# Optimization experiments

Measured on AMD Instinct MI355X. Metric: run time of the kernel, lower is better.

Reference implementation:

```python
import jax, jax.numpy as jnp
import numpy as np

N = 8192      # agent_num
F = 128       # feature dim
P = 16        # persona dim
E = 262144    # edges (N * avg_degree 32)


def setup_inputs() -> dict:
    key = jax.random.key(0)
    ks = jax.random.split(key, 10)
    return {
        "feature": jax.random.normal(ks[0], (N, F), dtype=jnp.float32),
        "next_feature": jax.random.normal(ks[1], (N, F), dtype=jnp.float32),
        "persona_t": jax.random.uniform(ks[2], (N, P), dtype=jnp.float32),
        "alpha": jax.random.normal(ks[3], (P,), dtype=jnp.float32),
        "beta": jax.random.normal(ks[4], (P,), dtype=jnp.float32),
        "gamma": jax.random.normal(ks[5], (P,), dtype=jnp.float32),
        "act_src": jax.random.randint(ks[6], (E,), 0, N, dtype=jnp.int32),
        "act_dst": jax.random.randint(ks[7], (E,), 0, N, dtype=jnp.int32),
        "edge_src": jax.random.randint(ks[8], (E,), 0, N, dtype=jnp.int32),
        "edge_dst": jax.random.randint(ks[9], (E,), 0, N, dtype=jnp.int32),
    }


def _row_l2_normalize(x):
    # norm_func: divide each row by its L2 norm (scatter-add of squares in torch)
    norms = jnp.sqrt(jnp.sum(x * x, axis=1, keepdims=True))
    return x / norms


def reference(feature, next_feature, persona_t, alpha, beta, gamma,
              act_src, act_dst, edge_src, edge_dst):
    n, f = feature.shape

    # ---- impact (gamma) path: adj_sim_self(next_action, old - new) ----
    diff = feature - next_feature                           # [N, F]
    # hadamard(adj, diff @ diff.T): only dot products on action edges
    impact_vals = jnp.sum(diff[act_src] * diff[act_dst], axis=1) / f   # [E]
    gamma_row = persona_t @ gamma                            # [N] persona-weighted gamma
    reward_impact = impact_vals * gamma_row[act_src]         # row-wise multiply

    # ---- similarity (alpha) path: adj_sim(next_action, norm(next_feature)) ----
    # step() normalizes next_feature, then adj_sim normalizes again (idempotent)
    nf = _row_l2_normalize(_row_l2_normalize(next_feature))  # [N, F]
    sim_vals = jnp.sum(nf[act_src] * nf[act_dst], axis=1)    # [E] cosine sims on edges
    alpha_row = persona_t @ alpha                            # [N]
    reward_sim = sim_vals * alpha_row[act_src]

    # ---- cost (beta) path: old edges (binary) * persona_beta broadcast over rows ----
    beta_row = persona_t @ beta                              # [N]
    reward_cost = beta_row[edge_src]                         # [E] (edge value = 1)

    # ---- reward = reward_sim - reward_cost + reward_impact on the union of supports ----
    reward = jnp.zeros((n, n), dtype=feature.dtype)
    reward = reward.at[act_src, act_dst].add(reward_sim + reward_impact)
    reward = reward.at[edge_src, edge_dst].add(-reward_cost)
    return reward
```

## Files before the change

### kernel.cpp

```cpp
#include <hip/hip_runtime.h>
#include <hip/hip_fp16.h>

#define N_AGENTS 8192
#define FDIM 128
#define PDIM 16
#define NEDGES 262144
#define CAP 128
#define OVERCAP 4096

typedef float floatx4 __attribute__((ext_vector_type(4)));
typedef int   intx2   __attribute__((ext_vector_type(2)));

__global__ __launch_bounds__(256) void row_prep_k(
        const float* __restrict__ feature,
        const float* __restrict__ next_feature,
        const float* __restrict__ persona,
        const float* __restrict__ alpha,
        const float* __restrict__ beta,
        const float* __restrict__ gamma,
        __half2* __restrict__ T2,
        float2* __restrict__ scale,
        float* __restrict__ brow,
        int* __restrict__ cnt,
        int* __restrict__ ocnt) {
    int row  = (blockIdx.x * blockDim.x + threadIdx.x) >> 6;
    int lane = threadIdx.x & 63;
    if (blockIdx.x == 0 && threadIdx.x == 0) *ocnt = 0;
    if (row >= N_AGENTS) return;

    const float2* f2 = (const float2*)(feature      + (size_t)row * FDIM);
    const float2* n2 = (const float2*)(next_feature + (size_t)row * FDIM);
    float2 f  = f2[lane];
    float2 nx = n2[lane];

    float2 d = make_float2(f.x - nx.x, f.y - nx.y);
    float ss = nx.x * nx.x + nx.y * nx.y;

    float pa = 0.f, pb = 0.f, pg = 0.f;
    if (lane < PDIM) {
        float p = persona[(size_t)row * PDIM + lane];
        pa = p * alpha[lane];
        pb = p * beta[lane];
        pg = p * gamma[lane];
    }

    #pragma unroll
    for (int off = 32; off > 0; off >>= 1) {
        ss += __shfl_xor(ss, off);
        pa += __shfl_xor(pa, off);
        pb += __shfl_xor(pb, off);
        pg += __shfl_xor(pg, off);
    }

    float inv = 1.0f / sqrtf(ss);
    __half2* trow = T2 + (size_t)row * 128;
    trow[lane]      = __float22half2_rn(make_float2(nx.x * inv, nx.y * inv));
    trow[64 + lane] = __float22half2_rn(d);

    if (lane == 0) {
        scale[row] = make_float2(pa, pg * (1.0f / FDIM));
        brow[row]  = pb;
        cnt[row]   = 0;
    }
}

__device__ inline float dot8(float4 a, float4 b) {
    const __half2* ha = (const __half2*)&a;
    const __half2* hb = (const __half2*)&b;
    float s = 0.f;
    #pragma unroll
    for (int j = 0; j < 4; ++j) {
        float2 fa = __half22float2(ha[j]);
        float2 fb = __half22float2(hb[j]);
        s += fa.x * fb.x + fa.y * fb.y;
    }
    return s;
}

__device__ inline void push_rec(int s, int d, float val,
                                int* cnt, intx2* bins,
                                int* ocnt, int4* olist) {
    int pos = atomicAdd(&cnt[s], 1);
    if (pos < CAP) {
        intx2 rec;
        rec.x = d;
        rec.y = __float_as_int(val);
        __builtin_nontemporal_store(rec, &bins[(size_t)s * CAP + pos]);
    } else {
        int op = atomicAdd(ocnt, 1);
        if (op < OVERCAP) olist[op] = make_int4(s, d, __float_as_int(val), 0);
    }
}

#define ACT_BLOCKS ((NEDGES * 16) / 256)
#define COST_BLOCKS (NEDGES / 256)
__global__ __launch_bounds__(256) void edge_bin_k(
        const int* __restrict__ asrc,
        const int* __restrict__ adst,
        const int* __restrict__ esrc,
        const int* __restrict__ edst,
        const __half* __restrict__ T,
        const float2* __restrict__ scale,
        const float* __restrict__ brow,
        int* __restrict__ cnt,
        intx2* __restrict__ bins,
        int* __restrict__ ocnt,
        int4* __restrict__ olist) {
    int b = blockIdx.x;
    if (b < ACT_BLOCKS) {
        int gid    = b * 256 + threadIdx.x;
        int e      = gid >> 4;
        int lane16 = gid & 15;
        int s = asrc[e];
        int d = adst[e];
        const float4* ts = (const float4*)(T + (size_t)s * 256);
        const float4* td = (const float4*)(T + (size_t)d * 256);
        int i0 = lane16 * 2;
        float acc = dot8(ts[i0], td[i0]) + dot8(ts[i0 + 1], td[i0 + 1]);
        acc += __shfl_xor(acc, 1, 16);
        acc += __shfl_xor(acc, 2, 16);
        acc += __shfl_xor(acc, 4, 16);
        float other = __shfl_xor(acc, 8, 16);
        if (lane16 == 0) {
            float2 sc = scale[s];
            float val = acc * sc.x + other * sc.y;
            push_rec(s, d, val, cnt, bins, ocnt, olist);
        }
    } else {
        int e = (b - ACT_BLOCKS) * 256 + threadIdx.x;
        int s = esrc[e];
        push_rec(s, edst[e], -brow[s], cnt, bins, ocnt, olist);
    }
}

__global__ __launch_bounds__(256) void row_assemble_k(
        const int* __restrict__ cnt,
        const intx2* __restrict__ bins,
        float* __restrict__ out) {
    __shared__ float rowbuf[N_AGENTS];
    int r   = blockIdx.x;
    int tid = threadIdx.x;

    floatx4* rb4 = (floatx4*)rowbuf;
    floatx4 z = (floatx4)0.f;
    #pragma unroll
    for (int i = 0; i < 8; ++i)
        rb4[tid + i * 256] = z;
    __syncthreads();

    int c = cnt[r];
    c = c < CAP ? c : CAP;
    for (int i = tid; i < c; i += 256) {
        intx2 rec = bins[(size_t)r * CAP + i];
        atomicAdd(&rowbuf[rec.x], __int_as_float(rec.y));
    }
    __syncthreads();

    floatx4* dst = (floatx4*)(out + (size_t)r * N_AGENTS);
    #pragma unroll
    for (int i = 0; i < 8; ++i)
        __builtin_nontemporal_store(rb4[tid + i * 256], &dst[tid + i * 256]);
}

__global__ __launch_bounds__(256) void overflow_k(
        const int* __restrict__ ocnt,
        const int4* __restrict__ olist,
        float* __restrict__ out) {
    int n = *ocnt;
    n = n < OVERCAP ? n : OVERCAP;
    for (int i = threadIdx.x; i < n; i += 256) {
        int4 rec = olist[i];
        atomicAdd(out + (size_t)rec.x * N_AGENTS + rec.y, __int_as_float(rec.z));
    }
}

extern "C" void kernel_launch(void* const* d_in, const int* in_sizes, int n_in,
                              void* d_out, int out_size, void* d_ws, size_t ws_size,
                              hipStream_t stream) {
    const float* feature      = (const float*)d_in[0];
    const float* next_feature = (const float*)d_in[1];
    const float* persona      = (const float*)d_in[2];
    const float* alpha        = (const float*)d_in[3];
    const float* beta         = (const float*)d_in[4];
    const float* gamma        = (const float*)d_in[5];
    const int*   act_src      = (const int*)d_in[6];
    const int*   act_dst      = (const int*)d_in[7];
    const int*   edge_src     = (const int*)d_in[8];
    const int*   edge_dst     = (const int*)d_in[9];

    float* out = (float*)d_out;

    char* ws = (char*)d_ws;
    __half* T     = (__half*)ws;                 ws += (size_t)N_AGENTS * 256 * sizeof(__half);
    float2* scale = (float2*)ws;                 ws += (size_t)N_AGENTS * sizeof(float2);
    float*  brow  = (float*)ws;                  ws += (size_t)N_AGENTS * sizeof(float);
    int*    cnt   = (int*)ws;                    ws += (size_t)N_AGENTS * sizeof(int);
    intx2*  bins  = (intx2*)ws;                  ws += (size_t)N_AGENTS * CAP * sizeof(intx2);
    int*    ocnt  = (int*)ws;                    ws += 16;
    int4*   olist = (int4*)ws;

    row_prep_k<<<N_AGENTS / 4, 256, 0, stream>>>(
        feature, next_feature, persona, alpha, beta, gamma,
        (__half2*)T, scale, brow, cnt, ocnt);

    edge_bin_k<<<ACT_BLOCKS + COST_BLOCKS, 256, 0, stream>>>(
        act_src, act_dst, edge_src, edge_dst,
        T, scale, brow, cnt, bins, ocnt, olist);

    row_assemble_k<<<N_AGENTS, 256, 0, stream>>>(cnt, bins, out);

    overflow_k<<<1, 256, 0, stream>>>(ocnt, olist, out);
}
```

Baseline: 338.2 us.

## Replace per-row binning and assembly with memset plus direct global atomics

Drops the per-source-row bucket scheme (counters, capped bins, overflow list, shared-memory row assembly). Edge values are now computed into a flat array, the 256MB output is cleared with hipMemsetAsync, and a scatter kernel atomically adds each action and cost edge straight into global memory. This removes the bin write/read traffic and the shared-memory assembly pass. In exchange it relies on the memset's write bandwidth and on scattered global float atomics over a large matrix.

```diff
diff --git a/kernel.cpp b/kernel.cpp
--- a/kernel.cpp
+++ b/kernel.cpp
@@ -5,11 +5,8 @@
 #define FDIM 128
 #define PDIM 16
 #define NEDGES 262144
-#define CAP 128
-#define OVERCAP 4096
 
 typedef float floatx4 __attribute__((ext_vector_type(4)));
-typedef int   intx2   __attribute__((ext_vector_type(2)));
 
 __global__ __launch_bounds__(256) void row_prep_k(
         const float* __restrict__ feature,
@@ -20,12 +17,9 @@
         const float* __restrict__ gamma,
         __half2* __restrict__ T2,
         float2* __restrict__ scale,
-        float* __restrict__ brow,
-        int* __restrict__ cnt,
-        int* __restrict__ ocnt) {
+        float* __restrict__ brow) {
     int row  = (blockIdx.x * blockDim.x + threadIdx.x) >> 6;
     int lane = threadIdx.x & 63;
-    if (blockIdx.x == 0 && threadIdx.x == 0) *ocnt = 0;
     if (row >= N_AGENTS) return;
 
     const float2* f2 = (const float2*)(feature      + (size_t)row * FDIM);
@@ -60,7 +54,6 @@
     if (lane == 0) {
         scale[row] = make_float2(pa, pg * (1.0f / FDIM));
         brow[row]  = pb;
-        cnt[row]   = 0;
     }
 }
 
@@ -77,100 +70,47 @@
     return s;
 }
 
-__device__ inline void push_rec(int s, int d, float val,
-                                int* cnt, intx2* bins,
-                                int* ocnt, int4* olist) {
-    int pos = atomicAdd(&cnt[s], 1);
-    if (pos < CAP) {
-        intx2 rec;
-        rec.x = d;
-        rec.y = __float_as_int(val);
-        __builtin_nontemporal_store(rec, &bins[(size_t)s * CAP + pos]);
-    } else {
-        int op = atomicAdd(ocnt, 1);
-        if (op < OVERCAP) olist[op] = make_int4(s, d, __float_as_int(val), 0);
+#define ACT_BLOCKS ((NEDGES * 16) / 256)
+__global__ __launch_bounds__(256) void act_val_k(
+        const int* __restrict__ asrc,
+        const int* __restrict__ adst,
+        const __half* __restrict__ T,
+        const float2* __restrict__ scale,
+        float* __restrict__ actval) {
+    int gid    = blockIdx.x * 256 + threadIdx.x;
+    int e      = gid >> 4;
+    int lane16 = gid & 15;
+    int s = asrc[e];
+    int d = adst[e];
+    const float4* ts = (const float4*)(T + (size_t)s * 256);
+    const float4* td = (const float4*)(T + (size_t)d * 256);
+    int i0 = lane16 * 2;
+    float acc = dot8(ts[i0], td[i0]) + dot8(ts[i0 + 1], td[i0 + 1]);
+    acc += __shfl_xor(acc, 1, 16);
+    acc += __shfl_xor(acc, 2, 16);
+    acc += __shfl_xor(acc, 4, 16);
+    float other = __shfl_xor(acc, 8, 16);
+    if (lane16 == 0) {
+        float2 sc = scale[s];
+        actval[e] = acc * sc.x + other * sc.y;
     }
 }
 
-#define ACT_BLOCKS ((NEDGES * 16) / 256)
-#define COST_BLOCKS (NEDGES / 256)
-__global__ __launch_bounds__(256) void edge_bin_k(
+__global__ __launch_bounds__(256) void scatter_k(
         const int* __restrict__ asrc,
         const int* __restrict__ adst,
+        const float* __restrict__ actval,
         const int* __restrict__ esrc,
         const int* __restrict__ edst,
-        const __half* __restrict__ T,
-        const float2* __restrict__ scale,
         const float* __restrict__ brow,
-        int* __restrict__ cnt,
-        intx2* __restrict__ bins,
-        int* __restrict__ ocnt,
-        int4* __restrict__ olist) {
-    int b = blockIdx.x;
-    if (b < ACT_BLOCKS) {
-        int gid    = b * 256 + threadIdx.x;
-        int e      = gid >> 4;
-        int lane16 = gid & 15;
-        int s = asrc[e];
-        int d = adst[e];
-        const float4* ts = (const float4*)(T + (size_t)s * 256);
-        const float4* td = (const float4*)(T + (size_t)d * 256);
-        int i0 = lane16 * 2;
-        float acc = dot8(ts[i0], td[i0]) + dot8(ts[i0 + 1], td[i0 + 1]);
-        acc += __shfl_xor(acc, 1, 16);
-        acc += __shfl_xor(acc, 2, 16);
-        acc += __shfl_xor(acc, 4, 16);
-        float other = __shfl_xor(acc, 8, 16);
-        if (lane16 == 0) {
-            float2 sc = scale[s];
-            float val = acc * sc.x + other * sc.y;
-            push_rec(s, d, val, cnt, bins, ocnt, olist);
-        }
+        float* __restrict__ out) {
+    int t = blockIdx.x * 256 + threadIdx.x;
+    if (t < NEDGES) {
+        atomicAdd(out + (size_t)asrc[t] * N_AGENTS + adst[t], actval[t]);
     } else {
-        int e = (b - ACT_BLOCKS) * 256 + threadIdx.x;
+        int e = t - NEDGES;
         int s = esrc[e];
-        push_rec(s, edst[e], -brow[s], cnt, bins, ocnt, olist);
-    }
-}
-
-__global__ __launch_bounds__(256) void row_assemble_k(
-        const int* __restrict__ cnt,
-        const intx2* __restrict__ bins,
-        float* __restrict__ out) {
-    __shared__ float rowbuf[N_AGENTS];
-    int r   = blockIdx.x;
-    int tid = threadIdx.x;
-
-    floatx4* rb4 = (floatx4*)rowbuf;
-    floatx4 z = (floatx4)0.f;
-    #pragma unroll
-    for (int i = 0; i < 8; ++i)
-        rb4[tid + i * 256] = z;
-    __syncthreads();
-
-    int c = cnt[r];
-    c = c < CAP ? c : CAP;
-    for (int i = tid; i < c; i += 256) {
-        intx2 rec = bins[(size_t)r * CAP + i];
-        atomicAdd(&rowbuf[rec.x], __int_as_float(rec.y));
-    }
-    __syncthreads();
-
-    floatx4* dst = (floatx4*)(out + (size_t)r * N_AGENTS);
-    #pragma unroll
-    for (int i = 0; i < 8; ++i)
-        __builtin_nontemporal_store(rb4[tid + i * 256], &dst[tid + i * 256]);
-}
-
-__global__ __launch_bounds__(256) void overflow_k(
-        const int* __restrict__ ocnt,
-        const int4* __restrict__ olist,
-        float* __restrict__ out) {
-    int n = *ocnt;
-    n = n < OVERCAP ? n : OVERCAP;
-    for (int i = threadIdx.x; i < n; i += 256) {
-        int4 rec = olist[i];
-        atomicAdd(out + (size_t)rec.x * N_AGENTS + rec.y, __int_as_float(rec.z));
+        atomicAdd(out + (size_t)s * N_AGENTS + edst[e], -brow[s]);
     }
 }
 
@@ -191,23 +131,20 @@
     float* out = (float*)d_out;
 
     char* ws = (char*)d_ws;
-    __half* T     = (__half*)ws;                 ws += (size_t)N_AGENTS * 256 * sizeof(__half);
-    float2* scale = (float2*)ws;                 ws += (size_t)N_AGENTS * sizeof(float2);
-    float*  brow  = (float*)ws;                  ws += (size_t)N_AGENTS * sizeof(float);
-    int*    cnt   = (int*)ws;                    ws += (size_t)N_AGENTS * sizeof(int);
-    intx2*  bins  = (intx2*)ws;                  ws += (size_t)N_AGENTS * CAP * sizeof(intx2);
-    int*    ocnt  = (int*)ws;                    ws += 16;
-    int4*   olist = (int4*)ws;
+    __half* T      = (__half*)ws;   ws += (size_t)N_AGENTS * 256 * sizeof(__half);
+    float2* scale  = (float2*)ws;   ws += (size_t)N_AGENTS * sizeof(float2);
+    float*  brow   = (float*)ws;    ws += (size_t)N_AGENTS * sizeof(float);
+    float*  actval = (float*)ws;
 
     row_prep_k<<<N_AGENTS / 4, 256, 0, stream>>>(
         feature, next_feature, persona, alpha, beta, gamma,
-        (__half2*)T, scale, brow, cnt, ocnt);
+        (__half2*)T, scale, brow);
 
-    edge_bin_k<<<ACT_BLOCKS + COST_BLOCKS, 256, 0, stream>>>(
-        act_src, act_dst, edge_src, edge_dst,
-        T, scale, brow, cnt, bins, ocnt, olist);
+    act_val_k<<<ACT_BLOCKS, 256, 0, stream>>>(
+        act_src, act_dst, T, scale, actval);
 
-    row_assemble_k<<<N_AGENTS, 256, 0, stream>>>(cnt, bins, out);
+    hipMemsetAsync(out, 0, (size_t)N_AGENTS * N_AGENTS * sizeof(float), stream);
 
-    overflow_k<<<1, 256, 0, stream>>>(ocnt, olist, out);
+    scatter_k<<<(2 * NEDGES) / 256, 256, 0, stream>>>(
+        act_src, act_dst, actval, edge_src, edge_dst, brow, out);
 }
```

Measured after the change: 357.0 us. +5.6%, slower.

## Move edge dot products into row assembly with split index-only bins

Applied to the files above, without the earlier changes.

Binning now stores only destination indices, in separate bins for action edges and cost edges, so the scatter pass no longer gathers features. The dot products run in the row-assembly kernel, where the source row of T is loaded once per block into registers and reused for all of that row's edges. The aim is to cut redundant source-row gathers and shrink bin records from 8 to 4 bytes. The cost is more work in the assembly kernel and a more complex overflow kernel that recomputes dot products on a single block.

```diff
diff --git a/kernel.cpp b/kernel.cpp
--- a/kernel.cpp
+++ b/kernel.cpp
@@ -9,7 +9,6 @@
 #define OVERCAP 4096
 
 typedef float floatx4 __attribute__((ext_vector_type(4)));
-typedef int   intx2   __attribute__((ext_vector_type(2)));
 
 __global__ __launch_bounds__(256) void row_prep_k(
         const float* __restrict__ feature,
@@ -21,7 +20,8 @@
         __half2* __restrict__ T2,
         float2* __restrict__ scale,
         float* __restrict__ brow,
-        int* __restrict__ cnt,
+        int* __restrict__ cntA,
+        int* __restrict__ cntC,
         int* __restrict__ ocnt) {
     int row  = (blockIdx.x * blockDim.x + threadIdx.x) >> 6;
     int lane = threadIdx.x & 63;
@@ -60,7 +60,8 @@
     if (lane == 0) {
         scale[row] = make_float2(pa, pg * (1.0f / FDIM));
         brow[row]  = pb;
-        cnt[row]   = 0;
+        cntA[row]  = 0;
+        cntC[row]  = 0;
     }
 }
 
@@ -77,83 +78,78 @@
     return s;
 }
 
-__device__ inline void push_rec(int s, int d, float val,
-                                int* cnt, intx2* bins,
-                                int* ocnt, int4* olist) {
-    int pos = atomicAdd(&cnt[s], 1);
-    if (pos < CAP) {
-        intx2 rec;
-        rec.x = d;
-        rec.y = __float_as_int(val);
-        __builtin_nontemporal_store(rec, &bins[(size_t)s * CAP + pos]);
-    } else {
-        int op = atomicAdd(ocnt, 1);
-        if (op < OVERCAP) olist[op] = make_int4(s, d, __float_as_int(val), 0);
-    }
-}
-
-#define ACT_BLOCKS ((NEDGES * 16) / 256)
-#define COST_BLOCKS (NEDGES / 256)
 __global__ __launch_bounds__(256) void edge_bin_k(
         const int* __restrict__ asrc,
         const int* __restrict__ adst,
         const int* __restrict__ esrc,
         const int* __restrict__ edst,
+        int* __restrict__ cntA,
+        int* __restrict__ cntC,
+        int* __restrict__ binsA,
+        int* __restrict__ binsC,
+        int* __restrict__ ocnt,
+        int4* __restrict__ olist) {
+    int t = blockIdx.x * 256 + threadIdx.x;
+    if (t < NEDGES) {
+        int s = asrc[t];
+        int d = adst[t];
+        int pos = atomicAdd(&cntA[s], 1);
+        if (pos < CAP) binsA[(size_t)s * CAP + pos] = d;
+        else { int op = atomicAdd(ocnt, 1); if (op < OVERCAP) olist[op] = make_int4(s, d, 0, 0); }
+    } else {
+        int e = t - NEDGES;
+        int s = esrc[e];
+        int d = edst[e];
+        int pos = atomicAdd(&cntC[s], 1);
+        if (pos < CAP) binsC[(size_t)s * CAP + pos] = d;
+        else { int op = atomicAdd(ocnt, 1); if (op < OVERCAP) olist[op] = make_int4(s, d, 1, 0); }
+    }
+}
+
+__global__ __launch_bounds__(256) void row_assemble_k(
+        const int* __restrict__ cntA,
+        const int* __restrict__ binsA,
+        const int* __restrict__ cntC,
+        const int* __restrict__ binsC,
         const __half* __restrict__ T,
         const float2* __restrict__ scale,
         const float* __restrict__ brow,
-        int* __restrict__ cnt,
-        intx2* __restrict__ bins,
-        int* __restrict__ ocnt,
-        int4* __restrict__ olist) {
-    int b = blockIdx.x;
-    if (b < ACT_BLOCKS) {
-        int gid    = b * 256 + threadIdx.x;
-        int e      = gid >> 4;
-        int lane16 = gid & 15;
-        int s = asrc[e];
-        int d = adst[e];
-        const float4* ts = (const float4*)(T + (size_t)s * 256);
+        float* __restrict__ out) {
+    __shared__ float rowbuf[N_AGENTS];
+    int r   = blockIdx.x;
+    int tid = threadIdx.x;
+
+    floatx4* rb4 = (floatx4*)rowbuf;
+    floatx4 z = (floatx4)0.f;
+    #pragma unroll
+    for (int i = 0; i < 8; ++i)
+        rb4[tid + i * 256] = z;
+
+    int grp    = tid >> 4;
+    int lane16 = tid & 15;
+    int i0     = lane16 * 2;
+    const float4* tr = (const float4*)(T + (size_t)r * 256);
+    float4 tsA = tr[i0];
+    float4 tsB = tr[i0 + 1];
+    float2 sc  = scale[r];
+    float  br  = brow[r];
+    int cA = cntA[r]; cA = cA < CAP ? cA : CAP;
+    int cC = cntC[r]; cC = cC < CAP ? cC : CAP;
+    __syncthreads();
+
+    for (int i = grp; i < cA; i += 16) {
+        int d = binsA[(size_t)r * CAP + i];
         const float4* td = (const float4*)(T + (size_t)d * 256);
-        int i0 = lane16 * 2;
-        float acc = dot8(ts[i0], td[i0]) + dot8(ts[i0 + 1], td[i0 + 1]);
+        float acc = dot8(tsA, td[i0]) + dot8(tsB, td[i0 + 1]);
         acc += __shfl_xor(acc, 1, 16);
         acc += __shfl_xor(acc, 2, 16);
         acc += __shfl_xor(acc, 4, 16);
         float other = __shfl_xor(acc, 8, 16);
-        if (lane16 == 0) {
-            float2 sc = scale[s];
-            float val = acc * sc.x + other * sc.y;
-            push_rec(s, d, val, cnt, bins, ocnt, olist);
-        }
-    } else {
-        int e = (b - ACT_BLOCKS) * 256 + threadIdx.x;
-        int s = esrc[e];
-        push_rec(s, edst[e], -brow[s], cnt, bins, ocnt, olist);
-    }
-}
-
-__global__ __launch_bounds__(256) void row_assemble_k(
-        const int* __restrict__ cnt,
-        const intx2* __restrict__ bins,
-        float* __restrict__ out) {
-    __shared__ float rowbuf[N_AGENTS];
-    int r   = blockIdx.x;
-    int tid = threadIdx.x;
-
-    floatx4* rb4 = (floatx4*)rowbuf;
-    floatx4 z = (floatx4)0.f;
-    #pragma unroll
-    for (int i = 0; i < 8; ++i)
-        rb4[tid + i * 256] = z;
-    __syncthreads();
-
-    int c = cnt[r];
-    c = c < CAP ? c : CAP;
-    for (int i = tid; i < c; i += 256) {
-        intx2 rec = bins[(size_t)r * CAP + i];
-        atomicAdd(&rowbuf[rec.x], __int_as_float(rec.y));
-    }
+        if (lane16 == 0)
+            atomicAdd(&rowbuf[d], acc * sc.x + other * sc.y);
+    }
+    for (int i = tid; i < cC; i += 256)
+        atomicAdd(&rowbuf[binsC[(size_t)r * CAP + i]], -br);
     __syncthreads();
 
     floatx4* dst = (floatx4*)(out + (size_t)r * N_AGENTS);
@@ -165,12 +161,34 @@
 __global__ __launch_bounds__(256) void overflow_k(
         const int* __restrict__ ocnt,
         const int4* __restrict__ olist,
+        const __half* __restrict__ T,
+        const float2* __restrict__ scale,
+        const float* __restrict__ brow,
         float* __restrict__ out) {
     int n = *ocnt;
     n = n < OVERCAP ? n : OVERCAP;
-    for (int i = threadIdx.x; i < n; i += 256) {
+    int grp    = threadIdx.x >> 4;
+    int lane16 = threadIdx.x & 15;
+    int i0     = lane16 * 2;
+    for (int i = grp; i < n; i += 16) {
         int4 rec = olist[i];
-        atomicAdd(out + (size_t)rec.x * N_AGENTS + rec.y, __int_as_float(rec.z));
+        if (rec.z) {
+            if (lane16 == 0)
+                atomicAdd(out + (size_t)rec.x * N_AGENTS + rec.y, -brow[rec.x]);
+        } else {
+            const float4* ts = (const float4*)(T + (size_t)rec.x * 256);
+            const float4* td = (const float4*)(T + (size_t)rec.y * 256);
+            float acc = dot8(ts[i0], td[i0]) + dot8(ts[i0 + 1], td[i0 + 1]);
+            acc += __shfl_xor(acc, 1, 16);
+            acc += __shfl_xor(acc, 2, 16);
+            acc += __shfl_xor(acc, 4, 16);
+            float other = __shfl_xor(acc, 8, 16);
+            if (lane16 == 0) {
+                float2 sc = scale[rec.x];
+                atomicAdd(out + (size_t)rec.x * N_AGENTS + rec.y,
+                          acc * sc.x + other * sc.y);
+            }
+        }
     }
 }
 
@@ -191,23 +209,26 @@
     float* out = (float*)d_out;
 
     char* ws = (char*)d_ws;
-    __half* T     = (__half*)ws;                 ws += (size_t)N_AGENTS * 256 * sizeof(__half);
-    float2* scale = (float2*)ws;                 ws += (size_t)N_AGENTS * sizeof(float2);
-    float*  brow  = (float*)ws;                  ws += (size_t)N_AGENTS * sizeof(float);
-    int*    cnt   = (int*)ws;                    ws += (size_t)N_AGENTS * sizeof(int);
-    intx2*  bins  = (intx2*)ws;                  ws += (size_t)N_AGENTS * CAP * sizeof(intx2);
-    int*    ocnt  = (int*)ws;                    ws += 16;
+    __half* T     = (__half*)ws;   ws += (size_t)N_AGENTS * 256 * sizeof(__half);
+    float2* scale = (float2*)ws;   ws += (size_t)N_AGENTS * sizeof(float2);
+    float*  brow  = (float*)ws;    ws += (size_t)N_AGENTS * sizeof(float);
+    int*    cntA  = (int*)ws;      ws += (size_t)N_AGENTS * sizeof(int);
+    int*    cntC  = (int*)ws;      ws += (size_t)N_AGENTS * sizeof(int);
+    int*    binsA = (int*)ws;      ws += (size_t)N_AGENTS * CAP * sizeof(int);
+    int*    binsC = (int*)ws;      ws += (size_t)N_AGENTS * CAP * sizeof(int);
+    int*    ocnt  = (int*)ws;      ws += 16;
     int4*   olist = (int4*)ws;
 
     row_prep_k<<<N_AGENTS / 4, 256, 0, stream>>>(
         feature, next_feature, persona, alpha, beta, gamma,
-        (__half2*)T, scale, brow, cnt, ocnt);
-
-    edge_bin_k<<<ACT_BLOCKS + COST_BLOCKS, 256, 0, stream>>>(
+        (__half2*)T, scale, brow, cntA, cntC, ocnt);
+
+    edge_bin_k<<<(2 * NEDGES) / 256, 256, 0, stream>>>(
         act_src, act_dst, edge_src, edge_dst,
-        T, scale, brow, cnt, bins, ocnt, olist);
-
-    row_assemble_k<<<N_AGENTS, 256, 0, stream>>>(cnt, bins, out);
-
-    overflow_k<<<1, 256, 0, stream>>>(ocnt, olist, out);
-}
+        cntA, cntC, binsA, binsC, ocnt, olist);
+
+    row_assemble_k<<<N_AGENTS, 256, 0, stream>>>(
+        cntA, binsA, cntC, binsC, T, scale, brow, out);
+
+    overflow_k<<<1, 256, 0, stream>>>(ocnt, olist, T, scale, brow, out);
+}
```

Result: no change. 331.6 us (-1.9%).
